# Optimization experiments

Hardware: AMD Instinct MI355X
Metric: run time of the kernel (lower is better)

The kernel has to match this reference:

```python
import jax, jax.numpy as jnp
from jax import lax
import numpy as np

SEQ, B, H = 512, 64, 1024


def setup_inputs() -> dict:
    key = jax.random.key(0)
    k1, k2, k3, k4, k5, k6 = jax.random.split(key, 6)
    hidden = jax.random.normal(k1, (SEQ, B, H), dtype=jnp.float32)
    problem_q = jax.random.normal(k2, (B, H), dtype=jnp.float32)
    s = 1.0 / np.sqrt(H)
    WK = jax.random.uniform(k3, (H, H), minval=-s, maxval=s, dtype=jnp.float32)
    bK = jax.random.uniform(k4, (H,), minval=-s, maxval=s, dtype=jnp.float32)
    WV = jax.random.uniform(k5, (H, H), minval=-s, maxval=s, dtype=jnp.float32)
    bV = jax.random.uniform(k6, (H,), minval=-s, maxval=s, dtype=jnp.float32)
    return {"num_xs": 8, "hidden": hidden, "problem_q": problem_q,
            "WK": WK, "bK": bK, "WV": WV, "bV": bV}


def reference(num_xs, hidden, problem_q, WK, bK, WV, bV):
    # hidden: [S, B, H] -> [B, S, H]
    h = jnp.transpose(hidden, (1, 0, 2))
    k = jnp.einsum('bsh,kh->bsk', h, WK) + bK   # K projection, [B, S, H]
    v = jnp.einsum('bsh,vh->bsv', h, WV) + bV   # V projection, [B, S, H]

    def step(x, _):
        # x: [B, H]; scores over seq positions
        scores = jnp.einsum('bh,bsh->bs', x, k)       # [B, S]
        attn = jax.nn.softmax(scores, axis=-1)
        nx = jnp.einsum('bs,bsh->bh', attn, v)        # [B, H]
        return nx, nx

    _, rest = lax.scan(step, problem_q, None, length=num_xs - 1)  # [num_xs-1, B, H]
    xs = jnp.concatenate([problem_q[None], rest], axis=0)          # [num_xs, B, H]
    return jnp.transpose(xs, (1, 0, 2))                            # [B, num_xs, H]
```

## Files before the change

### kernel.cpp

```cpp
#include <hip/hip_runtime.h>

#define SEQ   512
#define BATCH 64
#define HID   1024
#define NX    8
#define SG    8
#define SB    8
#define NBAT  8
#define YBB   2

__global__ __launch_bounds__(256) void init_kernel(
    const float* __restrict__ WV, const float* __restrict__ WK,
    const float* __restrict__ bV, float* __restrict__ WVT,
    float* __restrict__ WCp, float* __restrict__ bc)
{
    __shared__ float smem[2 * 32 * 68];
    const int bid = blockIdx.x;
    const int tid = threadIdx.x;

    if (bid < 1024) {
        float (*As)[68] = (float(*)[68])smem;
        float (*Bs)[68] = (float(*)[68])(smem + 32 * 68);
        const int ks  = bid >> 8;
        const int idx = bid & 255;
        const int nt = idx & 15, mt = idx >> 4;
        const int nx = tid & 15, my = tid >> 4;
        const int r = tid >> 3, c = (tid & 7) * 8;
        const int kbase = ks * 256;

        float acc[4][4] = {};
        float4 a0 = *(const float4*)(WV + (size_t)(kbase + r) * HID + mt * 64 + c);
        float4 a1 = *(const float4*)(WV + (size_t)(kbase + r) * HID + mt * 64 + c + 4);
        float4 b0 = *(const float4*)(WK + (size_t)(kbase + r) * HID + nt * 64 + c);
        float4 b1 = *(const float4*)(WK + (size_t)(kbase + r) * HID + nt * 64 + c + 4);

        for (int k0 = kbase; k0 < kbase + 256; k0 += 32) {
            *(float4*)&As[r][c]     = a0;
            *(float4*)&As[r][c + 4] = a1;
            *(float4*)&Bs[r][c]     = b0;
            *(float4*)&Bs[r][c + 4] = b1;
            __syncthreads();
            if (k0 + 32 < kbase + 256) {
                a0 = *(const float4*)(WV + (size_t)(k0 + 32 + r) * HID + mt * 64 + c);
                a1 = *(const float4*)(WV + (size_t)(k0 + 32 + r) * HID + mt * 64 + c + 4);
                b0 = *(const float4*)(WK + (size_t)(k0 + 32 + r) * HID + nt * 64 + c);
                b1 = *(const float4*)(WK + (size_t)(k0 + 32 + r) * HID + nt * 64 + c + 4);
            }
            #pragma unroll 8
            for (int kk = 0; kk < 32; kk++) {
                const float4 a = *(const float4*)&As[kk][my * 4];
                const float4 b = *(const float4*)&Bs[kk][nx * 4];
                acc[0][0] += a.x * b.x; acc[0][1] += a.x * b.y;
                acc[0][2] += a.x * b.z; acc[0][3] += a.x * b.w;
                acc[1][0] += a.y * b.x; acc[1][1] += a.y * b.y;
                acc[1][2] += a.y * b.z; acc[1][3] += a.y * b.w;
                acc[2][0] += a.z * b.x; acc[2][1] += a.z * b.y;
                acc[2][2] += a.z * b.z; acc[2][3] += a.z * b.w;
                acc[3][0] += a.w * b.x; acc[3][1] += a.w * b.y;
                acc[3][2] += a.w * b.z; acc[3][3] += a.w * b.w;
            }
            __syncthreads();
        }
        float* dst = WCp + (size_t)ks * HID * HID;
        const int m = mt * 64 + my * 4, n = nt * 64 + nx * 4;
        #pragma unroll
        for (int i = 0; i < 4; i++)
            *(float4*)(dst + (size_t)(m + i) * HID + n) = *(float4*)acc[i];
    } else if (bid < 2048) {
        float (*tile)[33] = (float(*)[33])smem;
        const int idx = bid - 1024;
        const int bx = (idx & 31) * 32, by = (idx >> 5) * 32;
        const int tx = tid & 31, ty = tid >> 5;
        #pragma unroll
        for (int r2 = ty; r2 < 32; r2 += 8)
            tile[r2][tx] = WV[(size_t)(by + r2) * HID + bx + tx];
        __syncthreads();
        #pragma unroll
        for (int r2 = ty; r2 < 32; r2 += 8)
            WVT[(size_t)(bx + r2) * HID + by + tx] = tile[tx][r2];
    } else {
        float* xs  = smem;
        float* red = smem + 1024;
        const int nc = bid - 2048;
        *(float4*)(xs + tid * 4) = *(const float4*)(bV + tid * 4);
        __syncthreads();
        const int nl = tid & 31, jg = tid >> 5;
        const int n = nc * 32 + nl;
        const float* __restrict__ wp = WK + (size_t)(jg * 128) * HID + n;
        const float* __restrict__ xr = xs + jg * 128;
        float acc = 0.f;
        #pragma unroll 8
        for (int jj = 0; jj < 128; jj++)
            acc += xr[jj] * wp[(size_t)jj * HID];
        red[jg * 32 + nl] = acc;
        __syncthreads();
        if (tid < 32) {
            float s = 0.f;
            #pragma unroll
            for (int g = 0; g < 8; g++) s += red[g * 32 + tid];
            bc[nc * 32 + tid] = s;
        }
    }
}

__global__ __launch_bounds__(256) void wcadd_kernel(
    const float* __restrict__ WCp, float* __restrict__ WC)
{
    const size_t i = ((size_t)blockIdx.x * 256 + threadIdx.x) * 4;
    const size_t S = (size_t)HID * HID;
    float4 a = *(const float4*)(WCp + i);
    float4 b = *(const float4*)(WCp + S + i);
    float4 c = *(const float4*)(WCp + 2 * S + i);
    float4 d = *(const float4*)(WCp + 3 * S + i);
    float4 o;
    o.x = (a.x + b.x) + (c.x + d.x);
    o.y = (a.y + b.y) + (c.y + d.y);
    o.z = (a.z + b.z) + (c.z + d.z);
    o.w = (a.w + b.w) + (c.w + d.w);
    *(float4*)(WC + i) = o;
}

__global__ __launch_bounds__(256) void y_kernel(
    const float* __restrict__ W, const float* __restrict__ q,
    const float* __restrict__ zp, const float* __restrict__ ml,
    const float* __restrict__ bc, float* __restrict__ zs_slot,
    float* __restrict__ y, int mode)
{
    __shared__ float xs[HID * YBB];
    __shared__ float red[8][32][YBB];
    const int nc = blockIdx.x, bg = blockIdx.y;
    const int b0 = bg * YBB;
    const int tid = threadIdx.x;

    if (mode == 0) {
        for (int h = tid; h < HID; h += 256) {
            #pragma unroll
            for (int bl = 0; bl < YBB; bl++)
                xs[h * YBB + bl] = q[(size_t)(b0 + bl) * HID + h];
        }
    } else {
        float es[YBB][SG], invL[YBB];
        #pragma unroll
        for (int bl = 0; bl < YBB; bl++) {
            const int b = b0 + bl;
            float M = -1e30f;
            #pragma unroll
            for (int g = 0; g < SG; g++) M = fmaxf(M, ml[b * 2 * SG + 2 * g]);
            float L = 0.f;
            #pragma unroll
            for (int g = 0; g < SG; g++) {
                es[bl][g] = __expf(ml[b * 2 * SG + 2 * g] - M);
                L += ml[b * 2 * SG + 2 * g + 1] * es[bl][g];
            }
            invL[bl] = 1.0f / L;
        }
        for (int h = tid; h < HID; h += 256) {
            #pragma unroll
            for (int bl = 0; bl < YBB; bl++) {
                const int b = b0 + bl;
                float s = 0.f;
                #pragma unroll
                for (int g = 0; g < SG; g++)
                    s += zp[((size_t)(b * SG + g)) * HID + h] * es[bl][g];
                s *= invL[bl];
                xs[h * YBB + bl] = s;
                if (nc == 0 && zs_slot) zs_slot[(size_t)b * HID + h] = s;
            }
        }
    }
    __syncthreads();

    const int nl = tid & 31, jg = tid >> 5;
    const int n = nc * 32 + nl;
    const float* __restrict__ wp = W + (size_t)(jg * 128) * HID + n;
    const float* __restrict__ xr = xs + jg * 128 * YBB;
    float accx = 0.f, accy = 0.f;
    #pragma unroll 8
    for (int jj = 0; jj < 128; jj++) {
        const float wv = wp[(size_t)jj * HID];
        const float2 x2 = *(const float2*)(xr + jj * YBB);
        accx += x2.x * wv; accy += x2.y * wv;
    }
    red[jg][nl][0] = accx;
    red[jg][nl][1] = accy;
    __syncthreads();
    if (tid < 32 * YBB) {
        const int nl2 = tid & 31, bl = tid >> 5;
        float s = 0.f;
        #pragma unroll
        for (int g = 0; g < 8; g++) s += red[g][nl2][bl];
        if (mode != 0) s += bc[nc * 32 + nl2];
        y[(size_t)(b0 + bl) * HID + nc * 32 + nl2] = s;
    }
}

__global__ __launch_bounds__(256) void fused_attn_kernel(
    const float* __restrict__ hidden, const float* __restrict__ y,
    float* __restrict__ zp, float* __restrict__ ml)
{
    const int sg = blockIdx.x, b = blockIdx.y;
    const int tid = threadIdx.x;
    const int lane = tid & 63, w = tid >> 6;
    const int h4 = tid * 4;

    __shared__ float part[4][SB];

    const float4 yv = *(const float4*)(y + (size_t)b * HID + h4);
    float m = -1e30f, l = 0.f;
    float4 acc = {0.f, 0.f, 0.f, 0.f};

    for (int bb = 0; bb < NBAT; bb++) {
        float4 hv[SB];
        float p[SB];
        #pragma unroll
        for (int r = 0; r < SB; r++) {
            const int s = sg * 64 + bb * SB + r;
            hv[r] = *(const float4*)(hidden + ((size_t)s * BATCH + b) * HID + h4);
            p[r] = hv[r].x * yv.x + hv[r].y * yv.y
                 + hv[r].z * yv.z + hv[r].w * yv.w;
        }
        #pragma unroll
        for (int r = 0; r < SB; r++) {
            float s = p[r];
            #pragma unroll
            for (int off = 32; off; off >>= 1) s += __shfl_xor(s, off);
            if (lane == 0) part[w][r] = s;
        }
        __syncthreads();
        float sc[SB], mb = -1e30f;
        #pragma unroll
        for (int r = 0; r < SB; r++) {
            sc[r] = part[0][r] + part[1][r] + part[2][r] + part[3][r];
            mb = fmaxf(mb, sc[r]);
        }
        __syncthreads();
        const float newm  = fmaxf(m, mb);
        const float scale = __expf(m - newm);
        l *= scale;
        acc.x *= scale; acc.y *= scale; acc.z *= scale; acc.w *= scale;
        #pragma unroll
        for (int r = 0; r < SB; r++) {
            const float we = __expf(sc[r] - newm);
            l += we;
            acc.x += we * hv[r].x; acc.y += we * hv[r].y;
            acc.z += we * hv[r].z; acc.w += we * hv[r].w;
        }
        m = newm;
    }
    *(float4*)(zp + ((size_t)(b * SG + sg)) * HID + h4) = acc;
    if (tid == 0) {
        ml[(b * SG + sg) * 2 + 0] = m;
        ml[(b * SG + sg) * 2 + 1] = l;
    }
}

__global__ __launch_bounds__(256) void final_gemm(
    const float* __restrict__ WVT, const float* __restrict__ zs,
    const float* __restrict__ zp, const float* __restrict__ ml,
    const float* __restrict__ q, const float* __restrict__ bV,
    float* __restrict__ out)
{
    __shared__ float zst[7][HID];
    __shared__ float red[8][7][32];
    const int nc = blockIdx.x, b = blockIdx.y;
    const int tid = threadIdx.x;

    float M = -1e30f;
    #pragma unroll
    for (int g = 0; g < SG; g++) M = fmaxf(M, ml[b * 2 * SG + 2 * g]);
    float es[SG], L = 0.f;
    #pragma unroll
    for (int g = 0; g < SG; g++) {
        es[g] = __expf(ml[b * 2 * SG + 2 * g] - M);
        L += ml[b * 2 * SG + 2 * g + 1] * es[g];
    }
    const float invL = 1.0f / L;

    for (int i = tid; i < 7 * HID; i += 256) {
        const int si = i >> 10;
        const int h  = i & (HID - 1);
        float v;
        if (si < 6) {
            v = zs[((size_t)si * BATCH + b) * HID + h];
        } else {
            v = 0.f;
            #pragma unroll
            for (int g = 0; g < SG; g++)
                v += zp[((size_t)(b * SG + g)) * HID + h] * es[g];
            v *= invL;
        }
        zst[si][h] = v;
    }
    __syncthreads();

    const int nl = tid & 31, hg = tid >> 5;
    const int n = nc * 32 + nl;
    const float* __restrict__ wp = WVT + (size_t)(hg * 128) * HID + n;
    float acc[7] = {};
    #pragma unroll 4
    for (int hh = 0; hh < 128; hh++) {
        const float wv = wp[(size_t)hh * HID];
        const int h = hg * 128 + hh;
        #pragma unroll
        for (int si = 0; si < 7; si++)
            acc[si] += zst[si][h] * wv;
    }
    #pragma unroll
    for (int si = 0; si < 7; si++) red[hg][si][nl] = acc[si];
    __syncthreads();

    if (tid < 224) {
        const int si = tid >> 5, nl2 = tid & 31;
        const int n2 = nc * 32 + nl2;
        float s = bV[n2];
        #pragma unroll
        for (int g = 0; g < 8; g++) s += red[g][si][nl2];
        out[((size_t)(b * NX + si + 1)) * HID + n2] = s;
    } else {
        const int nl2 = tid - 224;
        const int n2 = nc * 32 + nl2;
        out[((size_t)(b * NX)) * HID + n2] = q[(size_t)b * HID + n2];
    }
}

extern "C" void kernel_launch(void* const* d_in, const int* in_sizes, int n_in,
                              void* d_out, int out_size, void* d_ws, size_t ws_size,
                              hipStream_t stream)
{
    const float* hidden = (const float*)d_in[1];
    const float* q      = (const float*)d_in[2];
    const float* WK     = (const float*)d_in[3];
    const float* WV     = (const float*)d_in[5];
    const float* bV     = (const float*)d_in[6];
    float* out = (float*)d_out;

    char* ws = (char*)d_ws;
    float* WVT = (float*)(ws);
    float* WC  = (float*)(ws + (4  << 20));
    float* zp  = (float*)(ws + (8  << 20));
    float* zs  = (float*)(ws + (10 << 20));
    float* y   = (float*)(ws + (12 << 20));
    float* ml  = (float*)(ws + (12 << 20) + (256 << 10));
    float* bc  = (float*)(ws + (12 << 20) + (512 << 10));
    float* WCp = (float*)(ws + (16 << 20));

    init_kernel<<<2080, 256, 0, stream>>>(WV, WK, bV, WVT, WCp, bc);
    wcadd_kernel<<<(HID * HID) / (256 * 4), 256, 0, stream>>>(WCp, WC);

    for (int t = 1; t < NX; t++) {
        if (t == 1) {
            y_kernel<<<dim3(32, BATCH / YBB), 256, 0, stream>>>(
                WK, q, nullptr, nullptr, nullptr, nullptr, y, 0);
        } else {
            float* slot = zs + (size_t)(t - 2) * BATCH * HID;
            y_kernel<<<dim3(32, BATCH / YBB), 256, 0, stream>>>(
                WC, nullptr, zp, ml, bc, slot, y, 1);
        }
        fused_attn_kernel<<<dim3(SG, BATCH), 256, 0, stream>>>(
            hidden, y, zp, ml);
    }
    final_gemm<<<dim3(32, BATCH), 256, 0, stream>>>(
        WVT, zs, zp, ml, q, bV, out);
}
```

Measured before the change: 332.6 us.

## Fold WC reduction into first y kernel and prefetch hidden rows in attention

Removes the standalone wcadd launch and has extra blocks of a new y1_kernel perform the four-way partial-sum reduction of WC alongside the first y projection, saving one launch and letting the two jobs overlap. The y kernel loses its mode branch. The attention kernel now software-pipelines its hidden loads, fetching the next batch of 8 rows into registers while the current batch is reduced and accumulated. This raises register pressure in the attention kernel and adds blocks to the first projection grid.

```diff
diff --git a/kernel.cpp b/kernel.cpp
--- a/kernel.cpp
+++ b/kernel.cpp
@@ -103,28 +103,72 @@
     }
 }
 
-__global__ __launch_bounds__(256) void wcadd_kernel(
-    const float* __restrict__ WCp, float* __restrict__ WC)
-{
-    const size_t i = ((size_t)blockIdx.x * 256 + threadIdx.x) * 4;
-    const size_t S = (size_t)HID * HID;
-    float4 a = *(const float4*)(WCp + i);
-    float4 b = *(const float4*)(WCp + S + i);
-    float4 c = *(const float4*)(WCp + 2 * S + i);
-    float4 d = *(const float4*)(WCp + 3 * S + i);
-    float4 o;
-    o.x = (a.x + b.x) + (c.x + d.x);
-    o.y = (a.y + b.y) + (c.y + d.y);
-    o.z = (a.z + b.z) + (c.z + d.z);
-    o.w = (a.w + b.w) + (c.w + d.w);
-    *(float4*)(WC + i) = o;
+__global__ __launch_bounds__(256) void y1_kernel(
+    const float* __restrict__ WK, const float* __restrict__ q,
+    const float* __restrict__ WCp, float* __restrict__ WC,
+    float* __restrict__ y)
+{
+    __shared__ float xs[HID * YBB];
+    __shared__ float red[8][32][YBB];
+    const int bx = blockIdx.x, by = blockIdx.y;
+    const int tid = threadIdx.x;
+
+    if (by >= 32) {
+        const int idx = (by - 32) * 32 + bx;
+        const size_t S = (size_t)HID * HID;
+        #pragma unroll
+        for (int k = 0; k < 4; k++) {
+            const size_t i = ((size_t)idx * 1024 + k * 256 + tid) * 4;
+            float4 a = *(const float4*)(WCp + i);
+            float4 b = *(const float4*)(WCp + S + i);
+            float4 c = *(const float4*)(WCp + 2 * S + i);
+            float4 d = *(const float4*)(WCp + 3 * S + i);
+            float4 o;
+            o.x = (a.x + b.x) + (c.x + d.x);
+            o.y = (a.y + b.y) + (c.y + d.y);
+            o.z = (a.z + b.z) + (c.z + d.z);
+            o.w = (a.w + b.w) + (c.w + d.w);
+            *(float4*)(WC + i) = o;
+        }
+        return;
+    }
+
+    const int nc = bx, bg = by;
+    const int b0 = bg * YBB;
+    for (int h = tid; h < HID; h += 256) {
+        #pragma unroll
+        for (int bl = 0; bl < YBB; bl++)
+            xs[h * YBB + bl] = q[(size_t)(b0 + bl) * HID + h];
+    }
+    __syncthreads();
+
+    const int nl = tid & 31, jg = tid >> 5;
+    const int n = nc * 32 + nl;
+    const float* __restrict__ wp = WK + (size_t)(jg * 128) * HID + n;
+    const float* __restrict__ xr = xs + jg * 128 * YBB;
+    float accx = 0.f, accy = 0.f;
+    #pragma unroll 8
+    for (int jj = 0; jj < 128; jj++) {
+        const float wv = wp[(size_t)jj * HID];
+        const float2 x2 = *(const float2*)(xr + jj * YBB);
+        accx += x2.x * wv; accy += x2.y * wv;
+    }
+    red[jg][nl][0] = accx;
+    red[jg][nl][1] = accy;
+    __syncthreads();
+    if (tid < 32 * YBB) {
+        const int nl2 = tid & 31, bl = tid >> 5;
+        float s = 0.f;
+        #pragma unroll
+        for (int g = 0; g < 8; g++) s += red[g][nl2][bl];
+        y[(size_t)(b0 + bl) * HID + nc * 32 + nl2] = s;
+    }
 }
 
 __global__ __launch_bounds__(256) void y_kernel(
-    const float* __restrict__ W, const float* __restrict__ q,
-    const float* __restrict__ zp, const float* __restrict__ ml,
-    const float* __restrict__ bc, float* __restrict__ zs_slot,
-    float* __restrict__ y, int mode)
+    const float* __restrict__ W, const float* __restrict__ zp,
+    const float* __restrict__ ml, const float* __restrict__ bc,
+    float* __restrict__ zs_slot, float* __restrict__ y)
 {
     __shared__ float xs[HID * YBB];
     __shared__ float red[8][32][YBB];
@@ -132,40 +176,32 @@
     const int b0 = bg * YBB;
     const int tid = threadIdx.x;
 
-    if (mode == 0) {
-        for (int h = tid; h < HID; h += 256) {
-            #pragma unroll
-            for (int bl = 0; bl < YBB; bl++)
-                xs[h * YBB + bl] = q[(size_t)(b0 + bl) * HID + h];
-        }
-    } else {
-        float es[YBB][SG], invL[YBB];
+    float es[YBB][SG], invL[YBB];
+    #pragma unroll
+    for (int bl = 0; bl < YBB; bl++) {
+        const int b = b0 + bl;
+        float M = -1e30f;
+        #pragma unroll
+        for (int g = 0; g < SG; g++) M = fmaxf(M, ml[b * 2 * SG + 2 * g]);
+        float L = 0.f;
+        #pragma unroll
+        for (int g = 0; g < SG; g++) {
+            es[bl][g] = __expf(ml[b * 2 * SG + 2 * g] - M);
+            L += ml[b * 2 * SG + 2 * g + 1] * es[bl][g];
+        }
+        invL[bl] = 1.0f / L;
+    }
+    for (int h = tid; h < HID; h += 256) {
         #pragma unroll
         for (int bl = 0; bl < YBB; bl++) {
             const int b = b0 + bl;
-            float M = -1e30f;
-            #pragma unroll
-            for (int g = 0; g < SG; g++) M = fmaxf(M, ml[b * 2 * SG + 2 * g]);
-            float L = 0.f;
-            #pragma unroll
-            for (int g = 0; g < SG; g++) {
-                es[bl][g] = __expf(ml[b * 2 * SG + 2 * g] - M);
-                L += ml[b * 2 * SG + 2 * g + 1] * es[bl][g];
-            }
-            invL[bl] = 1.0f / L;
-        }
-        for (int h = tid; h < HID; h += 256) {
-            #pragma unroll
-            for (int bl = 0; bl < YBB; bl++) {
-                const int b = b0 + bl;
-                float s = 0.f;
-                #pragma unroll
-                for (int g = 0; g < SG; g++)
-                    s += zp[((size_t)(b * SG + g)) * HID + h] * es[bl][g];
-                s *= invL[bl];
-                xs[h * YBB + bl] = s;
-                if (nc == 0 && zs_slot) zs_slot[(size_t)b * HID + h] = s;
-            }
+            float s = 0.f;
+            #pragma unroll
+            for (int g = 0; g < SG; g++)
+                s += zp[((size_t)(b * SG + g)) * HID + h] * es[bl][g];
+            s *= invL[bl];
+            xs[h * YBB + bl] = s;
+            if (nc == 0 && zs_slot) zs_slot[(size_t)b * HID + h] = s;
         }
     }
     __syncthreads();
@@ -189,7 +225,7 @@
         float s = 0.f;
         #pragma unroll
         for (int g = 0; g < 8; g++) s += red[g][nl2][bl];
-        if (mode != 0) s += bc[nc * 32 + nl2];
+        s += bc[nc * 32 + nl2];
         y[(size_t)(b0 + bl) * HID + nc * 32 + nl2] = s;
     }
 }
@@ -209,16 +245,28 @@
     float m = -1e30f, l = 0.f;
     float4 acc = {0.f, 0.f, 0.f, 0.f};
 
+    const float* __restrict__ hb =
+        hidden + ((size_t)(sg * 64) * BATCH + b) * HID + h4;
+    const size_t rs = (size_t)BATCH * HID;
+
+    float4 hv[SB];
+    #pragma unroll
+    for (int r = 0; r < SB; r++)
+        hv[r] = *(const float4*)(hb + (size_t)r * rs);
+
+    #pragma unroll
     for (int bb = 0; bb < NBAT; bb++) {
-        float4 hv[SB];
+        float4 hn[SB];
+        if (bb + 1 < NBAT) {
+            #pragma unroll
+            for (int r = 0; r < SB; r++)
+                hn[r] = *(const float4*)(hb + (size_t)((bb + 1) * SB + r) * rs);
+        }
         float p[SB];
         #pragma unroll
-        for (int r = 0; r < SB; r++) {
-            const int s = sg * 64 + bb * SB + r;
-            hv[r] = *(const float4*)(hidden + ((size_t)s * BATCH + b) * HID + h4);
+        for (int r = 0; r < SB; r++)
             p[r] = hv[r].x * yv.x + hv[r].y * yv.y
                  + hv[r].z * yv.z + hv[r].w * yv.w;
-        }
         #pragma unroll
         for (int r = 0; r < SB; r++) {
             float s = p[r];
@@ -246,6 +294,10 @@
             acc.z += we * hv[r].z; acc.w += we * hv[r].w;
         }
         m = newm;
+        if (bb + 1 < NBAT) {
+            #pragma unroll
+            for (int r = 0; r < SB; r++) hv[r] = hn[r];
+        }
     }
     *(float4*)(zp + ((size_t)(b * SG + sg)) * HID + h4) = acc;
     if (tid == 0) {
@@ -345,16 +397,14 @@
     float* WCp = (float*)(ws + (16 << 20));
 
     init_kernel<<<2080, 256, 0, stream>>>(WV, WK, bV, WVT, WCp, bc);
-    wcadd_kernel<<<(HID * HID) / (256 * 4), 256, 0, stream>>>(WCp, WC);
 
     for (int t = 1; t < NX; t++) {
         if (t == 1) {
-            y_kernel<<<dim3(32, BATCH / YBB), 256, 0, stream>>>(
-                WK, q, nullptr, nullptr, nullptr, nullptr, y, 0);
+            y1_kernel<<<dim3(32, 40), 256, 0, stream>>>(WK, q, WCp, WC, y);
         } else {
             float* slot = zs + (size_t)(t - 2) * BATCH * HID;
             y_kernel<<<dim3(32, BATCH / YBB), 256, 0, stream>>>(
-                WC, nullptr, zp, ml, bc, slot, y, 1);
+                WC, zp, ml, bc, slot, y);
         }
         fused_attn_kernel<<<dim3(SG, BATCH), 256, 0, stream>>>(
             hidden, y, zp, ml);
```

Result: slower. 433.1 us (+30.2%).
